# Optimization experiments

Hardware: AMD Instinct MI355X
Metric: run time of the kernel (lower is better)

The kernel has to match this reference:

```python
import jax, jax.numpy as jnp
import numpy as np

B, H, S, D = 8, 8, 1024, 64
MAX_REL = 512
VOCAB = 2 * MAX_REL + 1  # 1025


def setup_inputs() -> dict:
    key = jax.random.key(0)
    kq, kk, kv, kwk, kwv = jax.random.split(key, 5)
    q = jax.random.normal(kq, (B, H, S, D), dtype=jnp.float32)
    k = jax.random.normal(kk, (B, H, S, D), dtype=jnp.float32)
    v = jax.random.normal(kv, (B, H, S, D), dtype=jnp.float32)
    W_rel_keys = jax.random.normal(kwk, (VOCAB, D), dtype=jnp.float32) * 0.02
    W_rel_vals = jax.random.normal(kwv, (VOCAB, D), dtype=jnp.float32) * 0.02
    # Clipped relative positions, shifted to [0, 2*MAX_REL]: rel[i, j] = clip(j - i) + MAX_REL
    idx = jnp.arange(S)
    rel_positions = (jnp.clip(idx[None, :] - idx[:, None], -MAX_REL, MAX_REL) + MAX_REL).astype(jnp.int32)
    # Causal mask: True where position should be masked (j > i)
    mask = jnp.triu(jnp.ones((S, S), dtype=bool), k=1)[None, None]  # (1,1,S,S)
    return {"q": q, "k": k, "v": v, "W_rel_keys": W_rel_keys,
            "W_rel_vals": W_rel_vals, "rel_positions": rel_positions, "mask": mask}


def reference(q, k, v, W_rel_keys, W_rel_vals, rel_positions, mask):
    # Embedding lookups: (S, S, D)
    rel_keys = W_rel_keys[rel_positions]
    rel_vals = W_rel_vals[rel_positions]
    # relative_attention(q, k, rel_keys, transpose=True):
    #   q @ k^T  +  per-query-position matmul with rel_keys
    logits = (jnp.einsum('bhid,bhjd->bhij', q, k)
              + jnp.einsum('bhid,ijd->bhij', q, rel_keys))  # (B,H,S,S); NOTE: no 1/sqrt(d) scaling, as in source
    logits = jnp.where(mask, -jnp.inf, logits)
    weights = jax.nn.softmax(logits, axis=-1)
    # dropout p=0.0 (eval) -> identity
    # relative_attention(weights, v, rel_vals, transpose=False)
    output = (jnp.einsum('bhij,bhjd->bhid', weights, v)
              + jnp.einsum('bhij,ijd->bhid', weights, rel_vals))  # (B,H,S,D)
    return (output, weights)
```

## Files before the change

### kernel.cpp

```cpp
#include <hip/hip_runtime.h>
#include <math.h>

#define SS 1024
#define DD 64
#define BH 64

typedef __attribute__((ext_vector_type(4))) float fx4;
typedef __attribute__((ext_vector_type(8))) short sx8;
typedef __attribute__((ext_vector_type(4))) short sx4;

__device__ __forceinline__ unsigned short f2bf(float x) {
  unsigned u = __builtin_bit_cast(unsigned, x);
  u += 0x7fffu + ((u >> 16) & 1u);
  return (unsigned short)(u >> 16);
}
__device__ __forceinline__ float bf2f(unsigned short h) {
  return __builtin_bit_cast(float, ((unsigned)h) << 16);
}

__global__ __launch_bounds__(256, 3) void k_fused(
    const float* __restrict__ q, const float* __restrict__ k,
    const float* __restrict__ v, const float* __restrict__ RK,
    const float* __restrict__ RV, float* __restrict__ W, float* __restrict__ O) {
  const int bid = (blockIdx.y << 4) | blockIdx.x;
  const int nb = ((bid & 7) << 7) | (bid >> 3);
  const int it = nb & 15, bh = nb >> 4;
  const int i0 = it << 6;

  __shared__ __align__(16) char smem[54272];
  __shared__ float rowInv[64];
  short* const sKh = (short*)smem;
  short* const sKl = (short*)(smem + 9216);
  short* const sRh = (short*)(smem + 18432);
  short* const vT  = (short*)smem;
  short* const rvT = (short*)(smem + 9216);
  short* const wA  = (short*)(smem + 26624);
  short* const wSk = (short*)(smem + 36864);

  const int t = threadIdx.x;
  const int lane = t & 63, mt = t >> 6, quad = lane >> 4, lc = lane & 15;

  {
    const int r = t >> 2, g = t & 3;
    float* Wrow = W + ((size_t)(bh * SS + i0 + r)) * SS;
    float4 z; z.x = z.y = z.z = z.w = 0.f;
    for (int j = (it + 1) * 64 + g * 4; j < SS; j += 16) *(float4*)(Wrow + j) = z;
  }

#pragma unroll
  for (int e = 0; e < 4; ++e) {
    const int rr = quad * 4 + e;
    const int rloc = mt * 16 + rr;
    const int du = 63 + lc - rr;
    const int us0 = du & 15;
    const int A = (du >> 4) - mt;
#pragma unroll
    for (int kk = 0; kk < 8; ++kk) {
      if (kk < A || kk > A + 3) wSk[rloc * 136 + us0 + 16 * kk] = 0;
    }
  }

  sx8 aQh[2], aQl[2];
  {
    const float* qrow = q + ((size_t)(bh * SS + i0 + mt * 16 + lc)) * DD;
#pragma unroll
    for (int ks = 0; ks < 2; ++ks) {
      const int koff = ks * 32 + quad * 8;
      const float4 x0 = *(const float4*)(qrow + koff);
      const float4 x1 = *(const float4*)(qrow + koff + 4);
      const float xs[8] = {x0.x, x0.y, x0.z, x0.w, x1.x, x1.y, x1.z, x1.w};
#pragma unroll
      for (int e = 0; e < 8; ++e) {
        const unsigned short hb = f2bf(xs[e]);
        aQh[ks][e] = (short)hb;
        aQl[ks][e] = (short)f2bf(xs[e] - bf2f(hb));
      }
    }
  }

  auto stageKRK = [&](const int j0) {
    for (int idx = t; idx < 1024; idx += 256) {
      const int row = idx >> 4, c4 = (idx & 15) * 4;
      const float4 x = *(const float4*)(k + ((size_t)(bh * SS + j0 + row)) * DD + c4);
      const float xs[4] = {x.x, x.y, x.z, x.w};
      sx4 h, l;
#pragma unroll
      for (int e = 0; e < 4; ++e) {
        const unsigned short hb = f2bf(xs[e]);
        h[e] = (short)hb;
        l[e] = (short)f2bf(xs[e] - bf2f(hb));
      }
      *(sx4*)&sKh[row * 72 + c4] = h;
      *(sx4*)&sKl[row * 72 + c4] = l;
    }
    const int pLo = j0 - i0 - 63 + 512;
    for (int idx = t; idx < 2048; idx += 256) {
      const int u = idx >> 4, c4 = (idx & 15) * 4;
      int p = pLo + u;
      p = p < 0 ? 0 : (p > 512 ? 512 : p);
      const float4 x = *(const float4*)(RK + (size_t)p * DD + c4);
      sx4 h;
      h[0] = (short)f2bf(x.x); h[1] = (short)f2bf(x.y);
      h[2] = (short)f2bf(x.z); h[3] = (short)f2bf(x.w);
      *(sx4*)&sRh[u * 72 + c4] = h;
    }
  };

  auto logitsTile = [&](fx4* accS1, fx4* accS2) {
#pragma unroll
    for (int ks = 0; ks < 2; ++ks) {
      const int koff = ks * 32 + quad * 8;
#pragma unroll
      for (int nt = 0; nt < 4; ++nt) {
        const sx8 bKh = *(const sx8*)&sKh[(nt * 16 + lc) * 72 + koff];
        const sx8 bKl = *(const sx8*)&sKl[(nt * 16 + lc) * 72 + koff];
        accS1[nt] = __builtin_amdgcn_mfma_f32_16x16x32_bf16(aQh[ks], bKh, accS1[nt], 0, 0, 0);
        accS1[nt] = __builtin_amdgcn_mfma_f32_16x16x32_bf16(aQl[ks], bKh, accS1[nt], 0, 0, 0);
        accS1[nt] = __builtin_amdgcn_mfma_f32_16x16x32_bf16(aQh[ks], bKl, accS1[nt], 0, 0, 0);
      }
#pragma unroll
      for (int s = 0; s < 5; ++s) {
        const sx8 bR = *(const sx8*)&sRh[((3 - mt + s) * 16 + lc) * 72 + koff];
        accS2[s] = __builtin_amdgcn_mfma_f32_16x16x32_bf16(aQh[ks], bR, accS2[s], 0, 0, 0);
      }
    }
  };

  const fx4 zz = {0.f, 0.f, 0.f, 0.f};

  float sAcc[4] = {0.f, 0.f, 0.f, 0.f};
  for (int jt = 0; jt <= it; ++jt) {
    const int j0 = jt * 64;
    if (jt) __syncthreads();
    stageKRK(j0);
    __syncthreads();
    fx4 accS1[4] = {zz, zz, zz, zz};
    fx4 accS2[5] = {zz, zz, zz, zz, zz};
    logitsTile(accS1, accS2);
#pragma unroll
    for (int nt = 0; nt < 4; ++nt) {
#pragma unroll
      for (int e = 0; e < 4; ++e) {
        const int rr = quad * 4 + e;
        const int du = 63 + lc - rr;
        const int srcLane = (lane & 48) | (du & 15);
        const float g0 = __shfl(accS2[nt][e], srcLane, 64);
        const float g1 = __shfl(accS2[nt + 1][e], srcLane, 64);
        const float val = accS1[nt][e] + (du < 64 ? g0 : g1);
        const int col = j0 + nt * 16 + lc;
        if (col <= i0 + mt * 16 + rr) sAcc[e] += __expf(val);
      }
    }
  }
#pragma unroll
  for (int off = 1; off <= 8; off <<= 1) {
#pragma unroll
    for (int e = 0; e < 4; ++e) sAcc[e] += __shfl_xor(sAcc[e], off, 64);
  }
  if (lc == 0) {
#pragma unroll
    for (int e = 0; e < 4; ++e) rowInv[mt * 16 + quad * 4 + e] = 1.f / sAcc[e];
  }
  __syncthreads();

  float rI[4];
#pragma unroll
  for (int e = 0; e < 4; ++e) rI[e] = rowInv[mt * 16 + quad * 4 + e];
  fx4 accO[4] = {zz, zz, zz, zz};

  for (int jt = 0; jt <= it; ++jt) {
    const int j0 = jt * 64;
    const int pLo = j0 - i0 - 63 + 512;
    if (jt) __syncthreads();
    stageKRK(j0);
    __syncthreads();
    fx4 accS1[4] = {zz, zz, zz, zz};
    fx4 accS2[5] = {zz, zz, zz, zz, zz};
    logitsTile(accS1, accS2);
    __syncthreads();

    for (int idx = t; idx < 1024; idx += 256) {
      const int jj = idx >> 4, d4 = (idx & 15) * 4;
      const float4 x4 = *(const float4*)(v + ((size_t)(bh * SS + j0 + jj)) * DD + d4);
      vT[(d4 + 0) * 72 + jj] = (short)f2bf(x4.x);
      vT[(d4 + 1) * 72 + jj] = (short)f2bf(x4.y);
      vT[(d4 + 2) * 72 + jj] = (short)f2bf(x4.z);
      vT[(d4 + 3) * 72 + jj] = (short)f2bf(x4.w);
    }
    for (int idx = t; idx < 2048; idx += 256) {
      const int u = idx >> 4, d4 = (idx & 15) * 4;
      int p = pLo + u;
      p = p < 0 ? 0 : (p > 512 ? 512 : p);
      const float4 x4 = *(const float4*)(RV + (size_t)p * DD + d4);
      rvT[(d4 + 0) * 136 + u] = (short)f2bf(x4.x);
      rvT[(d4 + 1) * 136 + u] = (short)f2bf(x4.y);
      rvT[(d4 + 2) * 136 + u] = (short)f2bf(x4.z);
      rvT[(d4 + 3) * 136 + u] = (short)f2bf(x4.w);
    }

#pragma unroll
    for (int nt = 0; nt < 4; ++nt) {
#pragma unroll
      for (int e = 0; e < 4; ++e) {
        const int rr = quad * 4 + e;
        const int du = 63 + lc - rr;
        const int srcLane = (lane & 48) | (du & 15);
        const float g0 = __shfl(accS2[nt][e], srcLane, 64);
        const float g1 = __shfl(accS2[nt + 1][e], srcLane, 64);
        const float val = accS1[nt][e] + (du < 64 ? g0 : g1);
        const int col = j0 + nt * 16 + lc;
        const int rowg = i0 + mt * 16 + rr;
        const float w = (col <= rowg) ? __expf(val) * rI[e] : 0.f;
        W[((size_t)(bh * SS + rowg)) * SS + col] = w;
        const unsigned short h = f2bf(w);
        wA[(mt * 16 + rr) * 72 + nt * 16 + lc] = (short)h;
        wSk[(mt * 16 + rr) * 136 + du + 16 * (nt - mt)] = (short)h;
      }
    }
    __syncthreads();

#pragma unroll
    for (int ks = 0; ks < 2; ++ks) {
      const int koff = ks * 32 + quad * 8;
      const sx8 aW = *(const sx8*)&wA[(mt * 16 + lc) * 72 + koff];
#pragma unroll
      for (int nt = 0; nt < 4; ++nt) {
        const sx8 bV = *(const sx8*)&vT[(nt * 16 + lc) * 72 + koff];
        accO[nt] = __builtin_amdgcn_mfma_f32_16x16x32_bf16(aW, bV, accO[nt], 0, 0, 0);
      }
    }
#pragma unroll
    for (int ks = 0; ks < 4; ++ks) {
      const int koff = ks * 32 + quad * 8;
      const sx8 aS = *(const sx8*)&wSk[(mt * 16 + lc) * 136 + koff];
#pragma unroll
      for (int nt = 0; nt < 4; ++nt) {
        const sx8 bR = *(const sx8*)&rvT[(nt * 16 + lc) * 136 + koff];
        accO[nt] = __builtin_amdgcn_mfma_f32_16x16x32_bf16(aS, bR, accO[nt], 0, 0, 0);
      }
    }
  }

#pragma unroll
  for (int nt = 0; nt < 4; ++nt) {
#pragma unroll
    for (int e = 0; e < 4; ++e) {
      O[((size_t)(bh * SS + i0 + mt * 16 + quad * 4 + e)) * DD + nt * 16 + lc] = accO[nt][e];
    }
  }
}

extern "C" void kernel_launch(void* const* d_in, const int* in_sizes, int n_in,
                              void* d_out, int out_size, void* d_ws, size_t ws_size,
                              hipStream_t stream) {
  const float* q = (const float*)d_in[0];
  const float* k = (const float*)d_in[1];
  const float* v = (const float*)d_in[2];
  const float* RK = (const float*)d_in[3];
  const float* RV = (const float*)d_in[4];

  float* O = (float*)d_out;
  float* W = (float*)d_out + (size_t)BH * SS * DD;

  k_fused<<<dim3(16, BH), 256, 0, stream>>>(q, k, v, RK, RV, W, O);
}
```

Baseline: 653.6 us.

## Drop softmax denominator pass; normalize output at end and rescale weights in second kernel

Removes the first pass that recomputed all logits only to get the softmax row sums. The kernel now writes unnormalized exp values to W, accumulates row sums on the fly, and scales the output accumulator by the inverse sum at the end. A new rescale kernel rereads and rewrites the lower-triangular part of W to normalize it, trading half the logit MFMA work for extra global-memory traffic on the large weights tensor. As before, no max is subtracted before the exponential.

```diff
diff --git a/kernel.cpp b/kernel.cpp
--- a/kernel.cpp
+++ b/kernel.cpp
@@ -28,7 +28,6 @@
   const int i0 = it << 6;
 
   __shared__ __align__(16) char smem[54272];
-  __shared__ float rowInv[64];
   short* const sKh = (short*)smem;
   short* const sKl = (short*)(smem + 9216);
   short* const sRh = (short*)(smem + 18432);
@@ -127,45 +126,7 @@
   };
 
   const fx4 zz = {0.f, 0.f, 0.f, 0.f};
-
   float sAcc[4] = {0.f, 0.f, 0.f, 0.f};
-  for (int jt = 0; jt <= it; ++jt) {
-    const int j0 = jt * 64;
-    if (jt) __syncthreads();
-    stageKRK(j0);
-    __syncthreads();
-    fx4 accS1[4] = {zz, zz, zz, zz};
-    fx4 accS2[5] = {zz, zz, zz, zz, zz};
-    logitsTile(accS1, accS2);
-#pragma unroll
-    for (int nt = 0; nt < 4; ++nt) {
-#pragma unroll
-      for (int e = 0; e < 4; ++e) {
-        const int rr = quad * 4 + e;
-        const int du = 63 + lc - rr;
-        const int srcLane = (lane & 48) | (du & 15);
-        const float g0 = __shfl(accS2[nt][e], srcLane, 64);
-        const float g1 = __shfl(accS2[nt + 1][e], srcLane, 64);
-        const float val = accS1[nt][e] + (du < 64 ? g0 : g1);
-        const int col = j0 + nt * 16 + lc;
-        if (col <= i0 + mt * 16 + rr) sAcc[e] += __expf(val);
-      }
-    }
-  }
-#pragma unroll
-  for (int off = 1; off <= 8; off <<= 1) {
-#pragma unroll
-    for (int e = 0; e < 4; ++e) sAcc[e] += __shfl_xor(sAcc[e], off, 64);
-  }
-  if (lc == 0) {
-#pragma unroll
-    for (int e = 0; e < 4; ++e) rowInv[mt * 16 + quad * 4 + e] = 1.f / sAcc[e];
-  }
-  __syncthreads();
-
-  float rI[4];
-#pragma unroll
-  for (int e = 0; e < 4; ++e) rI[e] = rowInv[mt * 16 + quad * 4 + e];
   fx4 accO[4] = {zz, zz, zz, zz};
 
   for (int jt = 0; jt <= it; ++jt) {
@@ -210,8 +171,9 @@
         const float val = accS1[nt][e] + (du < 64 ? g0 : g1);
         const int col = j0 + nt * 16 + lc;
         const int rowg = i0 + mt * 16 + rr;
-        const float w = (col <= rowg) ? __expf(val) * rI[e] : 0.f;
+        const float w = (col <= rowg) ? __expf(val) : 0.f;
         W[((size_t)(bh * SS + rowg)) * SS + col] = w;
+        sAcc[e] += w;
         const unsigned short h = f2bf(w);
         wA[(mt * 16 + rr) * 72 + nt * 16 + lc] = (short)h;
         wSk[(mt * 16 + rr) * 136 + du + 16 * (nt - mt)] = (short)h;
@@ -242,10 +204,43 @@
   }
 
 #pragma unroll
+  for (int off = 1; off <= 8; off <<= 1) {
+#pragma unroll
+    for (int e = 0; e < 4; ++e) sAcc[e] += __shfl_xor(sAcc[e], off, 64);
+  }
+  float rI[4];
+#pragma unroll
+  for (int e = 0; e < 4; ++e) rI[e] = 1.f / sAcc[e];
+
+#pragma unroll
   for (int nt = 0; nt < 4; ++nt) {
 #pragma unroll
     for (int e = 0; e < 4; ++e) {
-      O[((size_t)(bh * SS + i0 + mt * 16 + quad * 4 + e)) * DD + nt * 16 + lc] = accO[nt][e];
+      O[((size_t)(bh * SS + i0 + mt * 16 + quad * 4 + e)) * DD + nt * 16 + lc] =
+          accO[nt][e] * rI[e];
+    }
+  }
+}
+
+__global__ __launch_bounds__(256) void k_rescale(float* __restrict__ W) {
+  const int it = blockIdx.x, bh = blockIdx.y;
+  const int i0 = it << 6;
+  const int wv = threadIdx.x >> 6, lane = threadIdx.x & 63;
+  const int ncol = i0 + 64;
+  for (int rr = 0; rr < 16; ++rr) {
+    float* __restrict__ Wrow = W + ((size_t)(bh * SS + i0 + wv * 16 + rr)) * SS;
+    float s = 0.f;
+    for (int j = lane * 4; j < ncol; j += 256) {
+      const float4 x = *(const float4*)(Wrow + j);
+      s += (x.x + x.y) + (x.z + x.w);
+    }
+#pragma unroll
+    for (int off = 1; off < 64; off <<= 1) s += __shfl_xor(s, off, 64);
+    const float inv = 1.f / s;
+    for (int j = lane * 4; j < ncol; j += 256) {
+      float4 x = *(const float4*)(Wrow + j);
+      x.x *= inv; x.y *= inv; x.z *= inv; x.w *= inv;
+      *(float4*)(Wrow + j) = x;
     }
   }
 }
@@ -263,4 +258,5 @@
   float* W = (float*)d_out + (size_t)BH * SS * DD;
 
   k_fused<<<dim3(16, BH), 256, 0, stream>>>(q, k, v, RK, RV, W, O);
-}
+  k_rescale<<<dim3(16, BH), 256, 0, stream>>>(W);
+}
```

New measurement: 735.2 us. 1.12x slower.
